# Kernel optimization log

Measured on AMD Instinct MI355X. Metric: run time of the kernel, lower is better.

The kernel has to match this reference:

```python
import jax, jax.numpy as jnp
import numpy as np

B = 5                      # dat_sz hardcoded in module; kernel shapes force batch == 5
X_DIM = 4096
H_DIM = 4096
T_DIM = 4096
D_DIM = X_DIM // T_DIM     # = 1 (required so z_dim == t_dim broadcasts in reparameterize_nm)
L_DIM = D_DIM * (D_DIM + 1) // 2
Z_DIM = T_DIM * L_DIM      # = 4096


def _linear_params(key, din, dout):
    kw, kb = jax.random.split(key)
    W = jax.random.normal(kw, (din, dout), dtype=jnp.float32) / np.float32(np.sqrt(din))
    b = jax.random.normal(kb, (dout,), dtype=jnp.float32) * np.float32(0.01)
    return W, b


def setup_inputs() -> dict:
    key = jax.random.key(0)
    ks = jax.random.split(key, 20)
    inp = {}
    inp["x"] = jax.random.normal(ks[0], (B, X_DIM), dtype=jnp.float32)
    inp["eps_xi"] = jax.random.normal(ks[1], (B, T_DIM), dtype=jnp.float32)
    inp["eps_f"] = jax.random.normal(ks[2], (B, D_DIM), dtype=jnp.float32)
    inp["eps_z"] = jax.random.normal(ks[3], (B, Z_DIM), dtype=jnp.float32)
    inp["W1"], inp["b1"] = _linear_params(ks[4], X_DIM, H_DIM)
    inp["W11"], inp["b11"] = _linear_params(ks[5], H_DIM, T_DIM)
    inp["W12"], inp["b12"] = _linear_params(ks[6], H_DIM, T_DIM)
    inp["W2"], inp["b2"] = _linear_params(ks[7], D_DIM, H_DIM)
    inp["W21"], inp["b21"] = _linear_params(ks[8], H_DIM, Z_DIM)
    inp["W22"], inp["b22"] = _linear_params(ks[9], H_DIM, T_DIM)
    inp["W23"], inp["b23"] = _linear_params(ks[10], X_DIM + Z_DIM, H_DIM)
    inp["W24"], inp["b24"] = _linear_params(ks[11], H_DIM, T_DIM + D_DIM)
    inp["W25"], inp["b25"] = _linear_params(ks[12], H_DIM, T_DIM + D_DIM)
    inp["W3"], inp["b3"] = _linear_params(ks[13], Z_DIM, H_DIM)
    inp["W31"], inp["b31"] = _linear_params(ks[14], H_DIM, X_DIM)
    inp["W32"], inp["b32"] = _linear_params(ks[15], H_DIM, X_DIM)
    inp["s"] = jax.random.normal(ks[16], (B, T_DIM), dtype=jnp.float32)
    inp["t"] = jax.random.normal(ks[17], (B, D_DIM), dtype=jnp.float32)
    inp["sigma"] = jnp.asarray(0.01, dtype=jnp.float32)
    inp["w"] = jnp.ones((T_DIM,), dtype=jnp.float32) / np.float32(T_DIM)
    inp["dist"] = 1  # unused by forward (matches torch signature)
    return inp


def _ard_kernel(a, b, sigma, w):
    # K[i,j] = sigma^2 * exp(-0.5 * sum_d w_d (a_i,d - b_j,d)^2)
    # Vectorized replacement of the original O(B^2) Python double loop.
    d2 = (a[:, None, :] - b[None, :, :]) ** 2            # [B, B, T]
    return (sigma ** 2) * jnp.exp(-0.5 * jnp.einsum('ijt,t->ij', d2, w))


def reference(x, eps_xi, eps_f, eps_z,
              W1, b1, W11, b11, W12, b12,
              W2, b2, W21, b21, W22, b22,
              W23, b23, W24, b24, W25, b25,
              W3, b3, W31, b31, W32, b32,
              s, t, sigma, w, dist):
    relu = jax.nn.relu
    # encode_1
    h1 = relu(x @ W1 + b1)
    qxi_mean = h1 @ W11 + b11
    log_qxi_cov = h1 @ W12 + b12
    # reparameterize_nm
    xi = jnp.exp(0.5 * log_qxi_cov) * eps_xi + qxi_mean
    # reparameterize_gp (training branch)
    K_ss = _ard_kernel(s, s, sigma, w)                    # [5,5]
    K_xs = _ard_kernel(xi, s, sigma, w)                   # [5,5]
    kk_inv = K_xs @ jnp.linalg.inv(K_ss)                  # [5,5]
    qf_mean = kk_inv @ t                                  # [5,D]
    cov = _ard_kernel(xi, xi, sigma, w) - kk_inv @ _ard_kernel(s, xi, sigma, w)
    qf_cov = jnp.diag(cov)                                # [5]
    f = jnp.sqrt(qf_cov)[:, None] * eps_f + qf_mean       # [5,D]
    # encode_2
    h2 = relu(f @ W2 + b2)
    z_mean = h2 @ W21 + b21                               # [5,Z]
    z_cov = h2 @ W22 + b22                                # [5,T] (== Z since d_dim=1)
    z = jnp.exp(0.5 * z_cov) * eps_z + z_mean
    # encode_3
    h23 = relu(jnp.concatenate([x, z], axis=1) @ W23 + b23)
    r_mean = h23 @ W24 + b24                              # [5,T+D]
    r_cov = h23 @ W25 + b25
    # decode
    h3 = relu(z @ W3 + b3)
    x_mean = h3 @ W31 + b31
    x_cov = h3 @ W32 + b32
    # losses
    qf_cov2 = jnp.broadcast_to(qf_cov[:, None], (B, D_DIM))
    q_mean = jnp.concatenate([qxi_mean, qf_mean], axis=1)
    q_cov = jnp.concatenate([log_qxi_cov, jnp.log(qf_cov2)], axis=1)
    kld1 = 0.5 * jnp.sum(-z_cov - 1.0 + jnp.exp(z_cov) + z_mean ** 2) / B
    kld2 = 0.5 * jnp.sum(r_cov - q_cov - 1.0
                         + jnp.exp(q_cov - r_cov)
                         + (q_mean - r_mean) ** 2 * jnp.exp(-r_cov)) / B
    kld_loss = kld1 + kld2
    log_pi = jnp.log(jnp.asarray(np.pi, dtype=jnp.float32))
    nll_loss = 0.5 * jnp.sum(log_pi + x_cov + jnp.exp(-x_cov) * (x - x_mean) ** 2) / B
    return (kld_loss, nll_loss, z_mean, z_cov, x_mean, x_cov)
```

## Files before the change

### kernel.cpp

```cpp
#include <hip/hip_runtime.h>
#include <math.h>

#define B5 5
#define DX 4096
#define DT 4096
#define DR 4097

enum {
  WS_SUMS  = 0,
  WS_CNT_XI  = 3,
  WS_CNT_FIN = 4,
  WS_CNT_ARD = 5,
  WS_ZERO_END = 8,
  WS_ACT1  = 16,
  WS_ACT23 = WS_ACT1  + 20480,
  WS_ACT3  = WS_ACT23 + 20480,
  WS_QXI_F = WS_ACT3  + 20480,
  WS_LQC_F = WS_QXI_F + 20480,
  WS_XIV   = WS_LQC_F + 20480,
  WS_Z     = WS_XIV   + 20480,
  WS_KSS   = WS_Z     + 20480,
  WS_KXS   = WS_KSS + 32,
  WS_F     = WS_KXS + 32,
  WS_QFM   = WS_F   + 8,
  WS_QFC   = WS_QFM + 8,
  WS_PART  = 143472,
  WS_P_H1  = WS_PART,
  WS_P_QXI = WS_P_H1  + 1310720,
  WS_P_LQC = WS_P_QXI + 1310720,
  WS_P_ZM  = WS_P_LQC + 1310720,
  WS_P_ZC  = WS_P_ZM  + 1310720,
  WS_P_H23 = WS_P_ZC  + 1310720,
  WS_P_H3  = WS_P_H23 + 2621440,
  WS_P_RM  = WS_P_H3  + 1310720,
  WS_P_RC  = WS_P_RM  + 1311040,
  WS_P_XM  = WS_P_RC  + 1311040,
  WS_P_XC  = WS_P_XM  + 1310720,
  WS_END   = WS_P_XC  + 1310720
};

#define GCOLS 256
#define GK    64
#define WROWS 16

__device__ inline float wave_sum(float v) {
  #pragma unroll
  for (int o = 32; o > 0; o >>= 1) v += __shfl_down(v, o, 64);
  return v;
}

template<int PROLOG, int DUAL, int ALIGNED>
__device__ __forceinline__ void gemm5_body(
    float* sx, float* red, int bx, int by,
    const float* __restrict__ p0, const float* __restrict__ p1,
    const float* __restrict__ p2,
    const float* __restrict__ Wa, const float* __restrict__ Wb,
    float* __restrict__ Pa,       float* __restrict__ Pb,
    int din, int dout)
{
  const int tid  = threadIdx.x;
  const int lane = tid & 63;
  const int wv   = tid >> 6;
  const long i0  = (long)by * GK;
  const long r0  = i0 + (long)wv * WROWS;

  float* sw = sx + wv * 80;
  for (int t = lane; t < B5 * WROWS; t += 64) {
    int b  = t >> 4;
    int il = t & 15;
    int i  = (int)(r0 + il);
    float v;
    if (PROLOG == 0)      v = p0[(long)b * din + i];
    else if (PROLOG == 2) v = fmaxf(p0[b] * p1[i] + p2[i], 0.f);
    else                  v = (i < DX) ? p0[(long)b * DX + i] : p1[(long)b * DT + (i - DX)];
    sw[t] = v;
  }

  const long o0 = (long)bx * GCOLS + lane * 4;
  const bool c0 = (o0 < dout), c1 = (o0 + 1 < dout), c2 = (o0 + 2 < dout), c3 = (o0 + 3 < dout);

  float accA[B5][4] = {};
  float accB[B5][4] = {};
  const float* wa = Wa + r0 * dout + o0;
  const float* wb = DUAL ? (Wb + r0 * dout + o0) : nullptr;

  #pragma unroll 8
  for (int il = 0; il < WROWS; ++il) {
    float4 A, Bv;
    if (ALIGNED) {
      A = *(const float4*)wa;
      if (DUAL) Bv = *(const float4*)wb;
    } else {
      A.x = c0 ? wa[0] : 0.f; A.y = c1 ? wa[1] : 0.f;
      A.z = c2 ? wa[2] : 0.f; A.w = c3 ? wa[3] : 0.f;
      if (DUAL) {
        Bv.x = c0 ? wb[0] : 0.f; Bv.y = c1 ? wb[1] : 0.f;
        Bv.z = c2 ? wb[2] : 0.f; Bv.w = c3 ? wb[3] : 0.f;
      }
    }
    #pragma unroll
    for (int b = 0; b < B5; ++b) {
      float xv = sw[b * WROWS + il];
      accA[b][0] += xv * A.x;  accA[b][1] += xv * A.y;
      accA[b][2] += xv * A.z;  accA[b][3] += xv * A.w;
      if (DUAL) {
        accB[b][0] += xv * Bv.x; accB[b][1] += xv * Bv.y;
        accB[b][2] += xv * Bv.z; accB[b][3] += xv * Bv.w;
      }
    }
    wa += dout; if (DUAL) wb += dout;
  }

  const int NJ = DUAL ? 40 : 20;
  if (wv > 0) {
    float* rr = red + (long)(wv - 1) * NJ * 64 + lane;
    #pragma unroll
    for (int b = 0; b < B5; ++b)
      #pragma unroll
      for (int j = 0; j < 4; ++j) {
        rr[(b*4+j)*64] = accA[b][j];
        if (DUAL) rr[(20+b*4+j)*64] = accB[b][j];
      }
  }
  __syncthreads();
  if (wv == 0) {
    #pragma unroll
    for (int w2 = 0; w2 < 3; ++w2) {
      const float* rr = red + (long)w2 * NJ * 64 + lane;
      #pragma unroll
      for (int b = 0; b < B5; ++b)
        #pragma unroll
        for (int j = 0; j < 4; ++j) {
          accA[b][j] += rr[(b*4+j)*64];
          if (DUAL) accB[b][j] += rr[(20+b*4+j)*64];
        }
    }
    if (c0) {
      #pragma unroll
      for (int b = 0; b < B5; ++b) {
        float* pa = Pa + ((long)by * B5 + b) * dout + o0;
        if (ALIGNED) *(float4*)pa = make_float4(accA[b][0], accA[b][1], accA[b][2], accA[b][3]);
        else { pa[0] = accA[b][0]; if (c1) pa[1] = accA[b][1];
               if (c2) pa[2] = accA[b][2]; if (c3) pa[3] = accA[b][3]; }
        if (DUAL) {
          float* pb = Pb + ((long)by * B5 + b) * dout + o0;
          if (ALIGNED) *(float4*)pb = make_float4(accB[b][0], accB[b][1], accB[b][2], accB[b][3]);
          else { pb[0] = accB[b][0]; if (c1) pb[1] = accB[b][1];
                 if (c2) pb[2] = accB[b][2]; if (c3) pb[3] = accB[b][3]; }
        }
      }
    }
  }
}

template<int PROLOG, int DUAL, int ALIGNED>
__global__ __launch_bounds__(256) void gemm5(
    const float* __restrict__ p0, const float* __restrict__ p1,
    const float* __restrict__ p2,
    const float* __restrict__ Wa, const float* __restrict__ Wb,
    float* __restrict__ Pa,       float* __restrict__ Pb,
    int din, int dout)
{
  __shared__ float sx[4 * 80];
  __shared__ float red[3 * 40 * 64];
  gemm5_body<PROLOG, DUAL, ALIGNED>(sx, red, blockIdx.x, blockIdx.y,
      p0, p1, p2, Wa, Wb, Pa, Pb, din, dout);
}

__global__ __launch_bounds__(256) void gemm5_G46(
    const float* __restrict__ x,   const float* __restrict__ z,
    const float* __restrict__ W23, float* __restrict__ P23,
    const float* __restrict__ W3,  float* __restrict__ P3)
{
  __shared__ float sx[4 * 80];
  __shared__ float red[3 * 40 * 64];
  int id = blockIdx.x;
  if (id < 2048) {
    gemm5_body<3, 0, 1>(sx, red, id & 15, id >> 4, x, z, nullptr,
                        W23, nullptr, P23, nullptr, 8192, 4096);
  } else {
    id -= 2048;
    gemm5_body<0, 0, 1>(sx, red, id & 15, id >> 4, z, nullptr, nullptr,
                        W3, nullptr, P3, nullptr, 4096, 4096);
  }
}

__global__ __launch_bounds__(256) void gemm5_G57(
    const float* __restrict__ act23,
    const float* __restrict__ W24, const float* __restrict__ W25,
    float* __restrict__ PRM,       float* __restrict__ PRC,
    const float* __restrict__ act3,
    const float* __restrict__ W31, const float* __restrict__ W32,
    float* __restrict__ PXM,       float* __restrict__ PXC)
{
  __shared__ float sx[4 * 80];
  __shared__ float red[3 * 40 * 64];
  int id = blockIdx.x;
  if (id < 1088) {
    gemm5_body<0, 1, 0>(sx, red, id % 17, id / 17, act23, nullptr, nullptr,
                        W24, W25, PRM, PRC, 4096, 4097);
  } else {
    id -= 1088;
    gemm5_body<0, 1, 1>(sx, red, id & 15, id >> 4, act3, nullptr, nullptr,
                        W31, W32, PXM, PXC, 4096, 4096);
  }
}

__global__ __launch_bounds__(256) void k_act1(
    const float* __restrict__ P, const float* __restrict__ bias, float* __restrict__ act,
    float* __restrict__ ctrl)
{
  if (blockIdx.x == 0 && threadIdx.x < WS_ZERO_END) ctrl[threadIdx.x] = 0.f;
  int idx = blockIdx.x * 256 + threadIdx.x;
  int b = idx >> 12, col = idx & (DT - 1);
  const float* pp = P + (long)b * DT + col;
  float s = 0.f;
  #pragma unroll 8
  for (int ks = 0; ks < 64; ++ks) s += pp[(long)ks * (B5 * DT)];
  act[idx] = fmaxf(s + bias[col], 0.f);
}

__global__ __launch_bounds__(256) void k_act23(
    const float* __restrict__ P23, const float* __restrict__ b23, float* __restrict__ act23,
    const float* __restrict__ P3,  const float* __restrict__ b3,  float* __restrict__ act3)
{
  int idx = blockIdx.x * 256 + threadIdx.x;
  if (idx < B5 * DT) {
    int b = idx >> 12, col = idx & (DT - 1);
    const float* pp = P23 + (long)b * DT + col;
    float s = 0.f;
    #pragma unroll 8
    for (int ks = 0; ks < 128; ++ks) s += pp[(long)ks * (B5 * DT)];
    act23[idx] = fmaxf(s + b23[col], 0.f);
  } else {
    int j = idx - B5 * DT;
    int b = j >> 12, col = j & (DT - 1);
    const float* pp = P3 + (long)b * DT + col;
    float s = 0.f;
    #pragma unroll 8
    for (int ks = 0; ks < 64; ++ks) s += pp[(long)ks * (B5 * DT)];
    act3[j] = fmaxf(s + b3[col], 0.f);
  }
}

__global__ __launch_bounds__(256) void k_xiard(
    const float* __restrict__ Pq, const float* __restrict__ Pl,
    const float* __restrict__ b11, const float* __restrict__ b12,
    const float* __restrict__ eps_xi,
    const float* __restrict__ s,   const float* __restrict__ w,
    const float* __restrict__ sigma,
    const float* __restrict__ t_in, const float* __restrict__ eps_f,
    float* __restrict__ qf, float* __restrict__ lf, float* __restrict__ xiv,
    float* __restrict__ Kss, float* __restrict__ Kxs,
    int* __restrict__ cnt_xi, int* __restrict__ cnt_ard,
    float* __restrict__ fv, float* __restrict__ qfm, float* __restrict__ qfc)
{
  if (blockIdx.x < 80) {
    int idx = blockIdx.x * 256 + threadIdx.x;
    int b = idx >> 12, col = idx & (DT - 1);
    const float* pq = Pq + (long)b * DT + col;
    const float* pl = Pl + (long)b * DT + col;
    float sq = 0.f, sl = 0.f;
    #pragma unroll 8
    for (int ks = 0; ks < 64; ++ks) { sq += pq[(long)ks * (B5 * DT)]; sl += pl[(long)ks * (B5 * DT)]; }
    float qm = sq + b11[col];
    float lq = sl + b12[col];
    qf[idx] = qm; lf[idx] = lq;
    xiv[idx] = expf(0.5f * lq) * eps_xi[idx] + qm;
    __threadfence();
    __syncthreads();
    if (threadIdx.x == 0) atomicAdd(cnt_xi, 1);
    return;
  }

  const int bid = blockIdx.x - 80;
  const bool xs = (bid >= 25);
  int q = xs ? bid - 25 : bid;
  const int i = q / 5, j = q % 5;

  if (xs) {
    if (threadIdx.x == 0) { while (atomicAdd(cnt_xi, 0) < 80) {} }
    __syncthreads();
    __threadfence();
  }
  const float* aa = xs ? (xiv + (long)i * DT) : (s + (long)i * DT);
  const float* bb = s + (long)j * DT;

  float sum = 0.f;
  for (int t = threadIdx.x; t < DT; t += 256) {
    float d = aa[t] - bb[t];
    sum += w[t] * d * d;
  }
  sum = wave_sum(sum);
  __shared__ float red[4];
  int lane = threadIdx.x & 63, wv = threadIdx.x >> 6;
  if (lane == 0) red[wv] = sum;
  __syncthreads();

  if (threadIdx.x == 0) {
    float tot = red[0] + red[1] + red[2] + red[3];
    float sg = sigma[0];
    float K = sg * sg * expf(-0.5f * tot);
    (xs ? Kxs : Kss)[i * 5 + j] = K;
    __threadfence();
    int old = atomicAdd(cnt_ard, 1);
    if (old == 49) {
      __threadfence();
      double M[5][5], Inv[5][5];
      for (int a = 0; a < 5; ++a)
        for (int b = 0; b < 5; ++b) { M[a][b] = Kss[a * 5 + b]; Inv[a][b] = (a == b) ? 1.0 : 0.0; }
      for (int c = 0; c < 5; ++c) {
        int p = c; double best = fabs(M[c][c]);
        for (int r = c + 1; r < 5; ++r) if (fabs(M[r][c]) > best) { best = fabs(M[r][c]); p = r; }
        if (p != c)
          for (int k = 0; k < 5; ++k) {
            double tm = M[c][k]; M[c][k] = M[p][k]; M[p][k] = tm;
            tm = Inv[c][k]; Inv[c][k] = Inv[p][k]; Inv[p][k] = tm;
          }
        double piv = 1.0 / M[c][c];
        for (int k = 0; k < 5; ++k) { M[c][k] *= piv; Inv[c][k] *= piv; }
        for (int r = 0; r < 5; ++r) if (r != c) {
          double m = M[r][c];
          for (int k = 0; k < 5; ++k) { M[r][k] -= m * M[c][k]; Inv[r][k] -= m * Inv[c][k]; }
        }
      }
      double kk[5][5];
      for (int a = 0; a < 5; ++a)
        for (int b = 0; b < 5; ++b) {
          double acc = 0.0;
          for (int k = 0; k < 5; ++k) acc += (double)Kxs[a * 5 + k] * Inv[k][b];
          kk[a][b] = acc;
        }
      double sg2 = (double)sg * (double)sg;
      for (int a = 0; a < 5; ++a) {
        double qm = 0.0, qc = sg2;
        for (int b = 0; b < 5; ++b) { qm += kk[a][b] * (double)t_in[b]; qc -= kk[a][b] * (double)Kxs[a * 5 + b]; }
        if (qc < 1e-12) qc = 1e-12;
        qfm[a] = (float)qm;
        qfc[a] = (float)qc;
        fv[a]  = sqrtf((float)qc) * eps_f[a] + (float)qm;
      }
    }
  }
}

__global__ __launch_bounds__(256) void k_z(
    const float* __restrict__ Pm, const float* __restrict__ Pc,
    const float* __restrict__ b21, const float* __restrict__ b22,
    const float* __restrict__ eps_z,
    float* __restrict__ out_zm, float* __restrict__ out_zc,
    float* __restrict__ zv, float* __restrict__ kld1sum)
{
  int idx = blockIdx.x * 256 + threadIdx.x;
  float term = 0.f;
  if (idx < B5 * DT) {
    int b = idx >> 12, col = idx & (DT - 1);
    const float* pm = Pm + (long)b * DT + col;
    const float* pc = Pc + (long)b * DT + col;
    float sm = 0.f, sc = 0.f;
    #pragma unroll 8
    for (int ks = 0; ks < 64; ++ks) { sm += pm[(long)ks * (B5 * DT)]; sc += pc[(long)ks * (B5 * DT)]; }
    float zm = sm + b21[col];
    float zc = sc + b22[col];
    out_zm[idx] = zm; out_zc[idx] = zc;
    zv[idx] = expf(0.5f * zc) * eps_z[idx] + zm;
    term = -zc - 1.f + expf(zc) + zm * zm;
  }
  term = wave_sum(term);
  if ((threadIdx.x & 63) == 0) atomicAdd(kld1sum, term);
}

__global__ __launch_bounds__(256) void k_fin(
    const float* __restrict__ Prm, const float* __restrict__ Prc,
    const float* __restrict__ b24, const float* __restrict__ b25,
    const float* __restrict__ qxi, const float* __restrict__ lqc,
    const float* __restrict__ qfm, const float* __restrict__ qfc,
    const float* __restrict__ Pxm, const float* __restrict__ Pxc,
    const float* __restrict__ b31, const float* __restrict__ b32,
    const float* __restrict__ x,
    float* __restrict__ out_xm, float* __restrict__ out_xc,
    float* __restrict__ sums, int* __restrict__ cnt, float* __restrict__ out01)
{
  const int gtid = blockIdx.x * 256 + threadIdx.x;
  float t2 = 0.f, t3 = 0.f;
  if (gtid < B5 * DR) {
    int b = gtid / DR, col = gtid % DR;
    const float* pm = Prm + (long)b * DR + col;
    const float* pc = Prc + (long)b * DR + col;
    float sm = 0.f, sc = 0.f;
    #pragma unroll 8
    for (int ks = 0; ks < 64; ++ks) { sm += pm[(long)ks * (B5 * DR)]; sc += pc[(long)ks * (B5 * DR)]; }
    float rm = sm + b24[col];
    float rc = sc + b25[col];
    float qm, qc;
    if (col < DT) { qm = qxi[(long)b * DT + col]; qc = lqc[(long)b * DT + col]; }
    else          { qm = qfm[b]; qc = logf(qfc[b]); }
    float d = qm - rm;
    t2 = rc - qc - 1.f + expf(qc - rc) + d * d * expf(-rc);
  } else {
    int idx = gtid - B5 * DR;
    if (idx < B5 * DX) {
      int b = idx >> 12, col = idx & (DX - 1);
      const float* pm = Pxm + (long)b * DX + col;
      const float* pc = Pxc + (long)b * DX + col;
      float sm = 0.f, sc = 0.f;
      #pragma unroll 8
      for (int ks = 0; ks < 64; ++ks) { sm += pm[(long)ks * (B5 * DX)]; sc += pc[(long)ks * (B5 * DX)]; }
      float xm = sm + b31[col];
      float xc = sc + b32[col];
      out_xm[idx] = xm; out_xc[idx] = xc;
      float d = x[idx] - xm;
      t3 = 1.14472988584940017f + xc + expf(-xc) * d * d;
    }
  }
  t2 = wave_sum(t2);
  t3 = wave_sum(t3);
  if ((threadIdx.x & 63) == 0) {
    if (t2 != 0.f) atomicAdd(&sums[1], t2);
    if (t3 != 0.f) atomicAdd(&sums[2], t3);
  }
  __syncthreads();
  if (threadIdx.x == 0) {
    __threadfence();
    int old = atomicAdd(cnt, 1);
    if (old == (int)gridDim.x - 1) {
      __threadfence();
      out01[0] = 0.5f * (sums[0] + sums[1]) / (float)B5;
      out01[1] = 0.5f * sums[2] / (float)B5;
    }
  }
}

extern "C" void kernel_launch(void* const* d_in, const int* in_sizes, int n_in,
                              void* d_out, int out_size, void* d_ws, size_t ws_size,
                              hipStream_t stream)
{
  const float* x      = (const float*)d_in[0];
  const float* eps_xi = (const float*)d_in[1];
  const float* eps_f  = (const float*)d_in[2];
  const float* eps_z  = (const float*)d_in[3];
  const float* W1  = (const float*)d_in[4];  const float* b1  = (const float*)d_in[5];
  const float* W11 = (const float*)d_in[6];  const float* b11 = (const float*)d_in[7];
  const float* W12 = (const float*)d_in[8];  const float* b12 = (const float*)d_in[9];
  const float* W2  = (const float*)d_in[10]; const float* b2  = (const float*)d_in[11];
  const float* W21 = (const float*)d_in[12]; const float* b21 = (const float*)d_in[13];
  const float* W22 = (const float*)d_in[14]; const float* b22 = (const float*)d_in[15];
  const float* W23 = (const float*)d_in[16]; const float* b23 = (const float*)d_in[17];
  const float* W24 = (const float*)d_in[18]; const float* b24 = (const float*)d_in[19];
  const float* W25 = (const float*)d_in[20]; const float* b25 = (const float*)d_in[21];
  const float* W3  = (const float*)d_in[22]; const float* b3  = (const float*)d_in[23];
  const float* W31 = (const float*)d_in[24]; const float* b31 = (const float*)d_in[25];
  const float* W32 = (const float*)d_in[26]; const float* b32 = (const float*)d_in[27];
  const float* s     = (const float*)d_in[28];
  const float* t     = (const float*)d_in[29];
  const float* sigma = (const float*)d_in[30];
  const float* w     = (const float*)d_in[31];

  float* ws  = (float*)d_ws;
  float* out = (float*)d_out;

  dim3 blk(256);

  gemm5<0,0,1><<<dim3(16,64), blk, 0, stream>>>(
      x, nullptr, nullptr, W1, nullptr, ws + WS_P_H1, nullptr, 4096, 4096);
  k_act1<<<80, blk, 0, stream>>>(ws + WS_P_H1, b1, ws + WS_ACT1, ws);
  gemm5<0,1,1><<<dim3(16,64), blk, 0, stream>>>(
      ws + WS_ACT1, nullptr, nullptr, W11, W12, ws + WS_P_QXI, ws + WS_P_LQC, 4096, 4096);
  k_xiard<<<130, blk, 0, stream>>>(
      ws + WS_P_QXI, ws + WS_P_LQC, b11, b12, eps_xi,
      s, w, sigma, t, eps_f,
      ws + WS_QXI_F, ws + WS_LQC_F, ws + WS_XIV,
      ws + WS_KSS, ws + WS_KXS,
      (int*)(ws + WS_CNT_XI), (int*)(ws + WS_CNT_ARD),
      ws + WS_F, ws + WS_QFM, ws + WS_QFC);
  gemm5<2,1,1><<<dim3(16,64), blk, 0, stream>>>(
      ws + WS_F, W2, b2, W21, W22, ws + WS_P_ZM, ws + WS_P_ZC, 4096, 4096);
  k_z<<<80, blk, 0, stream>>>(
      ws + WS_P_ZM, ws + WS_P_ZC, b21, b22, eps_z,
      out + 2, out + 2 + 20480, ws + WS_Z, ws + WS_SUMS);
  gemm5_G46<<<3072, blk, 0, stream>>>(
      x, ws + WS_Z, W23, ws + WS_P_H23, W3, ws + WS_P_H3);
  k_act23<<<160, blk, 0, stream>>>(
      ws + WS_P_H23, b23, ws + WS_ACT23, ws + WS_P_H3, b3, ws + WS_ACT3);
  gemm5_G57<<<2112, blk, 0, stream>>>(
      ws + WS_ACT23, W24, W25, ws + WS_P_RM, ws + WS_P_RC,
      ws + WS_ACT3,  W31, W32, ws + WS_P_XM, ws + WS_P_XC);
  k_fin<<<161, blk, 0, stream>>>(
      ws + WS_P_RM, ws + WS_P_RC, b24, b25,
      ws + WS_QXI_F, ws + WS_LQC_F,
      ws + WS_QFM, ws + WS_QFC,
      ws + WS_P_XM, ws + WS_P_XC, b31, b32, x,
      out + 2 + 40960, out + 2 + 61440,
      ws + WS_SUMS, (int*)(ws + WS_CNT_FIN), out);
}
```

Before: 257.5 us.

## Retile GEMV kernels to 16-row K slices with wider column tiles

Restructures the skinny batch-5 GEMM kernels. Each block now covers 16 K rows and 512 output columns, with each of the four waves owning 128 columns via float2 loads, instead of splitting K across waves and reducing through shared memory. This removes the LDS cross-wave reduction and its sync, and doubles the grid size. The cost is four times as many split-K partial sums, so the workspace grows and the downstream reduce kernels must read 256 or 512 partials per output instead of 64, which adds substantial memory traffic.

```diff
diff --git a/kernel.cpp b/kernel.cpp
--- a/kernel.cpp
+++ b/kernel.cpp
@@ -26,22 +26,21 @@
   WS_QFC   = WS_QFM + 8,
   WS_PART  = 143472,
   WS_P_H1  = WS_PART,
-  WS_P_QXI = WS_P_H1  + 1310720,
-  WS_P_LQC = WS_P_QXI + 1310720,
-  WS_P_ZM  = WS_P_LQC + 1310720,
-  WS_P_ZC  = WS_P_ZM  + 1310720,
-  WS_P_H23 = WS_P_ZC  + 1310720,
-  WS_P_H3  = WS_P_H23 + 2621440,
-  WS_P_RM  = WS_P_H3  + 1310720,
-  WS_P_RC  = WS_P_RM  + 1311040,
-  WS_P_XM  = WS_P_RC  + 1311040,
-  WS_P_XC  = WS_P_XM  + 1310720,
-  WS_END   = WS_P_XC  + 1310720
+  WS_P_QXI = WS_P_H1  + 5242880,
+  WS_P_LQC = WS_P_QXI + 5242880,
+  WS_P_ZM  = WS_P_LQC + 5242880,
+  WS_P_ZC  = WS_P_ZM  + 5242880,
+  WS_P_H23 = WS_P_ZC  + 5242880,
+  WS_P_H3  = WS_P_H23 + 10485760,
+  WS_P_RM  = WS_P_H3  + 5242880,
+  WS_P_RC  = WS_P_RM  + 5244160,
+  WS_P_XM  = WS_P_RC  + 5244160,
+  WS_P_XC  = WS_P_XM  + 5242880,
+  WS_END   = WS_P_XC  + 5242880
 };
 
-#define GCOLS 256
-#define GK    64
-#define WROWS 16
+#define GCOLS 512
+#define GK    16
 
 __device__ inline float wave_sum(float v) {
   #pragma unroll
@@ -51,7 +50,7 @@
 
 template<int PROLOG, int DUAL, int ALIGNED>
 __device__ __forceinline__ void gemm5_body(
-    float* sx, float* red, int bx, int by,
+    float* sx, int bx, int by,
     const float* __restrict__ p0, const float* __restrict__ p1,
     const float* __restrict__ p2,
     const float* __restrict__ Wa, const float* __restrict__ Wb,
@@ -62,92 +61,56 @@
   const int lane = tid & 63;
   const int wv   = tid >> 6;
   const long i0  = (long)by * GK;
-  const long r0  = i0 + (long)wv * WROWS;
-
-  float* sw = sx + wv * 80;
-  for (int t = lane; t < B5 * WROWS; t += 64) {
-    int b  = t >> 4;
-    int il = t & 15;
-    int i  = (int)(r0 + il);
+
+  if (tid < B5 * GK) {
+    int b  = tid >> 4;
+    int il = tid & 15;
+    int i  = (int)i0 + il;
     float v;
     if (PROLOG == 0)      v = p0[(long)b * din + i];
     else if (PROLOG == 2) v = fmaxf(p0[b] * p1[i] + p2[i], 0.f);
     else                  v = (i < DX) ? p0[(long)b * DX + i] : p1[(long)b * DT + (i - DX)];
-    sw[t] = v;
-  }
-
-  const long o0 = (long)bx * GCOLS + lane * 4;
-  const bool c0 = (o0 < dout), c1 = (o0 + 1 < dout), c2 = (o0 + 2 < dout), c3 = (o0 + 3 < dout);
-
-  float accA[B5][4] = {};
-  float accB[B5][4] = {};
-  const float* wa = Wa + r0 * dout + o0;
-  const float* wb = DUAL ? (Wb + r0 * dout + o0) : nullptr;
+    sx[b * GK + il] = v;
+  }
+  __syncthreads();
+
+  const long o0 = (long)bx * GCOLS + wv * 128 + lane * 2;
+  const bool c0 = (o0 < dout), c1 = (o0 + 1 < dout);
+
+  float accA[B5][2] = {};
+  float accB[B5][2] = {};
+  const float* wa = Wa + i0 * dout + o0;
+  const float* wb = DUAL ? (Wb + i0 * dout + o0) : nullptr;
 
   #pragma unroll 8
-  for (int il = 0; il < WROWS; ++il) {
-    float4 A, Bv;
+  for (int il = 0; il < GK; ++il) {
+    float w0a, w1a, w0b = 0.f, w1b = 0.f;
     if (ALIGNED) {
-      A = *(const float4*)wa;
-      if (DUAL) Bv = *(const float4*)wb;
+      float2 ta = *(const float2*)wa; w0a = ta.x; w1a = ta.y;
+      if (DUAL) { float2 tb = *(const float2*)wb; w0b = tb.x; w1b = tb.y; }
     } else {
-      A.x = c0 ? wa[0] : 0.f; A.y = c1 ? wa[1] : 0.f;
-      A.z = c2 ? wa[2] : 0.f; A.w = c3 ? wa[3] : 0.f;
-      if (DUAL) {
-        Bv.x = c0 ? wb[0] : 0.f; Bv.y = c1 ? wb[1] : 0.f;
-        Bv.z = c2 ? wb[2] : 0.f; Bv.w = c3 ? wb[3] : 0.f;
-      }
+      w0a = c0 ? wa[0] : 0.f; w1a = c1 ? wa[1] : 0.f;
+      if (DUAL) { w0b = c0 ? wb[0] : 0.f; w1b = c1 ? wb[1] : 0.f; }
     }
     #pragma unroll
     for (int b = 0; b < B5; ++b) {
-      float xv = sw[b * WROWS + il];
-      accA[b][0] += xv * A.x;  accA[b][1] += xv * A.y;
-      accA[b][2] += xv * A.z;  accA[b][3] += xv * A.w;
+      float xv = sx[b * GK + il];
+      accA[b][0] += xv * w0a; accA[b][1] += xv * w1a;
+      if (DUAL) { accB[b][0] += xv * w0b; accB[b][1] += xv * w1b; }
+    }
+    wa += dout; if (DUAL) wb += dout;
+  }
+
+  if (c0) {
+    #pragma unroll
+    for (int b = 0; b < B5; ++b) {
+      float* pa = Pa + ((long)by * B5 + b) * dout + o0;
+      if (ALIGNED) *(float2*)pa = make_float2(accA[b][0], accA[b][1]);
+      else { pa[0] = accA[b][0]; if (c1) pa[1] = accA[b][1]; }
       if (DUAL) {
-        accB[b][0] += xv * Bv.x; accB[b][1] += xv * Bv.y;
-        accB[b][2] += xv * Bv.z; accB[b][3] += xv * Bv.w;
-      }
-    }
-    wa += dout; if (DUAL) wb += dout;
-  }
-
-  const int NJ = DUAL ? 40 : 20;
-  if (wv > 0) {
-    float* rr = red + (long)(wv - 1) * NJ * 64 + lane;
-    #pragma unroll
-    for (int b = 0; b < B5; ++b)
-      #pragma unroll
-      for (int j = 0; j < 4; ++j) {
-        rr[(b*4+j)*64] = accA[b][j];
-        if (DUAL) rr[(20+b*4+j)*64] = accB[b][j];
-      }
-  }
-  __syncthreads();
-  if (wv == 0) {
-    #pragma unroll
-    for (int w2 = 0; w2 < 3; ++w2) {
-      const float* rr = red + (long)w2 * NJ * 64 + lane;
-      #pragma unroll
-      for (int b = 0; b < B5; ++b)
-        #pragma unroll
-        for (int j = 0; j < 4; ++j) {
-          accA[b][j] += rr[(b*4+j)*64];
-          if (DUAL) accB[b][j] += rr[(20+b*4+j)*64];
-        }
-    }
-    if (c0) {
-      #pragma unroll
-      for (int b = 0; b < B5; ++b) {
-        float* pa = Pa + ((long)by * B5 + b) * dout + o0;
-        if (ALIGNED) *(float4*)pa = make_float4(accA[b][0], accA[b][1], accA[b][2], accA[b][3]);
-        else { pa[0] = accA[b][0]; if (c1) pa[1] = accA[b][1];
-               if (c2) pa[2] = accA[b][2]; if (c3) pa[3] = accA[b][3]; }
-        if (DUAL) {
-          float* pb = Pb + ((long)by * B5 + b) * dout + o0;
-          if (ALIGNED) *(float4*)pb = make_float4(accB[b][0], accB[b][1], accB[b][2], accB[b][3]);
-          else { pb[0] = accB[b][0]; if (c1) pb[1] = accB[b][1];
-                 if (c2) pb[2] = accB[b][2]; if (c3) pb[3] = accB[b][3]; }
-        }
+        float* pb = Pb + ((long)by * B5 + b) * dout + o0;
+        if (ALIGNED) *(float2*)pb = make_float2(accB[b][0], accB[b][1]);
+        else { pb[0] = accB[b][0]; if (c1) pb[1] = accB[b][1]; }
       }
     }
   }
@@ -161,9 +124,8 @@
     float* __restrict__ Pa,       float* __restrict__ Pb,
     int din, int dout)
 {
-  __shared__ float sx[4 * 80];
-  __shared__ float red[3 * 40 * 64];
-  gemm5_body<PROLOG, DUAL, ALIGNED>(sx, red, blockIdx.x, blockIdx.y,
+  __shared__ float sx[B5 * GK];
+  gemm5_body<PROLOG, DUAL, ALIGNED>(sx, blockIdx.x, blockIdx.y,
       p0, p1, p2, Wa, Wb, Pa, Pb, din, dout);
 }
 
@@ -172,15 +134,14 @@
     const float* __restrict__ W23, float* __restrict__ P23,
     const float* __restrict__ W3,  float* __restrict__ P3)
 {
-  __shared__ float sx[4 * 80];
-  __shared__ float red[3 * 40 * 64];
+  __shared__ float sx[B5 * GK];
   int id = blockIdx.x;
-  if (id < 2048) {
-    gemm5_body<3, 0, 1>(sx, red, id & 15, id >> 4, x, z, nullptr,
+  if (id < 4096) {
+    gemm5_body<3, 0, 1>(sx, id & 7, id >> 3, x, z, nullptr,
                         W23, nullptr, P23, nullptr, 8192, 4096);
   } else {
-    id -= 2048;
-    gemm5_body<0, 0, 1>(sx, red, id & 15, id >> 4, z, nullptr, nullptr,
+    id -= 4096;
+    gemm5_body<0, 0, 1>(sx, id & 7, id >> 3, z, nullptr, nullptr,
                         W3, nullptr, P3, nullptr, 4096, 4096);
   }
 }
@@ -193,15 +154,14 @@
     const float* __restrict__ W31, const float* __restrict__ W32,
     float* __restrict__ PXM,       float* __restrict__ PXC)
 {
-  __shared__ float sx[4 * 80];
-  __shared__ float red[3 * 40 * 64];
+  __shared__ float sx[B5 * GK];
   int id = blockIdx.x;
-  if (id < 1088) {
-    gemm5_body<0, 1, 0>(sx, red, id % 17, id / 17, act23, nullptr, nullptr,
+  if (id < 2304) {
+    gemm5_body<0, 1, 0>(sx, id % 9, id / 9, act23, nullptr, nullptr,
                         W24, W25, PRM, PRC, 4096, 4097);
   } else {
-    id -= 1088;
-    gemm5_body<0, 1, 1>(sx, red, id & 15, id >> 4, act3, nullptr, nullptr,
+    id -= 2304;
+    gemm5_body<0, 1, 1>(sx, id & 7, id >> 3, act3, nullptr, nullptr,
                         W31, W32, PXM, PXC, 4096, 4096);
   }
 }
@@ -216,7 +176,7 @@
   const float* pp = P + (long)b * DT + col;
   float s = 0.f;
   #pragma unroll 8
-  for (int ks = 0; ks < 64; ++ks) s += pp[(long)ks * (B5 * DT)];
+  for (int ks = 0; ks < 256; ++ks) s += pp[(long)ks * (B5 * DT)];
   act[idx] = fmaxf(s + bias[col], 0.f);
 }
 
@@ -230,7 +190,7 @@
     const float* pp = P23 + (long)b * DT + col;
     float s = 0.f;
     #pragma unroll 8
-    for (int ks = 0; ks < 128; ++ks) s += pp[(long)ks * (B5 * DT)];
+    for (int ks = 0; ks < 512; ++ks) s += pp[(long)ks * (B5 * DT)];
     act23[idx] = fmaxf(s + b23[col], 0.f);
   } else {
     int j = idx - B5 * DT;
@@ -238,7 +198,7 @@
     const float* pp = P3 + (long)b * DT + col;
     float s = 0.f;
     #pragma unroll 8
-    for (int ks = 0; ks < 64; ++ks) s += pp[(long)ks * (B5 * DT)];
+    for (int ks = 0; ks < 256; ++ks) s += pp[(long)ks * (B5 * DT)];
     act3[j] = fmaxf(s + b3[col], 0.f);
   }
 }
@@ -262,7 +222,7 @@
     const float* pl = Pl + (long)b * DT + col;
     float sq = 0.f, sl = 0.f;
     #pragma unroll 8
-    for (int ks = 0; ks < 64; ++ks) { sq += pq[(long)ks * (B5 * DT)]; sl += pl[(long)ks * (B5 * DT)]; }
+    for (int ks = 0; ks < 256; ++ks) { sq += pq[(long)ks * (B5 * DT)]; sl += pl[(long)ks * (B5 * DT)]; }
     float qm = sq + b11[col];
     float lq = sl + b12[col];
     qf[idx] = qm; lf[idx] = lq;
@@ -359,7 +319,7 @@
     const float* pc = Pc + (long)b * DT + col;
     float sm = 0.f, sc = 0.f;
     #pragma unroll 8
-    for (int ks = 0; ks < 64; ++ks) { sm += pm[(long)ks * (B5 * DT)]; sc += pc[(long)ks * (B5 * DT)]; }
+    for (int ks = 0; ks < 256; ++ks) { sm += pm[(long)ks * (B5 * DT)]; sc += pc[(long)ks * (B5 * DT)]; }
     float zm = sm + b21[col];
     float zc = sc + b22[col];
     out_zm[idx] = zm; out_zc[idx] = zc;
@@ -389,7 +349,7 @@
     const float* pc = Prc + (long)b * DR + col;
     float sm = 0.f, sc = 0.f;
     #pragma unroll 8
-    for (int ks = 0; ks < 64; ++ks) { sm += pm[(long)ks * (B5 * DR)]; sc += pc[(long)ks * (B5 * DR)]; }
+    for (int ks = 0; ks < 256; ++ks) { sm += pm[(long)ks * (B5 * DR)]; sc += pc[(long)ks * (B5 * DR)]; }
     float rm = sm + b24[col];
     float rc = sc + b25[col];
     float qm, qc;
@@ -405,7 +365,7 @@
       const float* pc = Pxc + (long)b * DX + col;
       float sm = 0.f, sc = 0.f;
       #pragma unroll 8
-      for (int ks = 0; ks < 64; ++ks) { sm += pm[(long)ks * (B5 * DX)]; sc += pc[(long)ks * (B5 * DX)]; }
+      for (int ks = 0; ks < 256; ++ks) { sm += pm[(long)ks * (B5 * DX)]; sc += pc[(long)ks * (B5 * DX)]; }
       float xm = sm + b31[col];
       float xc = sc + b32[col];
       out_xm[idx] = xm; out_xc[idx] = xc;
@@ -461,10 +421,10 @@
 
   dim3 blk(256);
 
-  gemm5<0,0,1><<<dim3(16,64), blk, 0, stream>>>(
+  gemm5<0,0,1><<<dim3(8,256), blk, 0, stream>>>(
       x, nullptr, nullptr, W1, nullptr, ws + WS_P_H1, nullptr, 4096, 4096);
   k_act1<<<80, blk, 0, stream>>>(ws + WS_P_H1, b1, ws + WS_ACT1, ws);
-  gemm5<0,1,1><<<dim3(16,64), blk, 0, stream>>>(
+  gemm5<0,1,1><<<dim3(8,256), blk, 0, stream>>>(
       ws + WS_ACT1, nullptr, nullptr, W11, W12, ws + WS_P_QXI, ws + WS_P_LQC, 4096, 4096);
   k_xiard<<<130, blk, 0, stream>>>(
       ws + WS_P_QXI, ws + WS_P_LQC, b11, b12, eps_xi,
@@ -473,16 +433,16 @@
       ws + WS_KSS, ws + WS_KXS,
       (int*)(ws + WS_CNT_XI), (int*)(ws + WS_CNT_ARD),
       ws + WS_F, ws + WS_QFM, ws + WS_QFC);
-  gemm5<2,1,1><<<dim3(16,64), blk, 0, stream>>>(
+  gemm5<2,1,1><<<dim3(8,256), blk, 0, stream>>>(
       ws + WS_F, W2, b2, W21, W22, ws + WS_P_ZM, ws + WS_P_ZC, 4096, 4096);
   k_z<<<80, blk, 0, stream>>>(
       ws + WS_P_ZM, ws + WS_P_ZC, b21, b22, eps_z,
       out + 2, out + 2 + 20480, ws + WS_Z, ws + WS_SUMS);
-  gemm5_G46<<<3072, blk, 0, stream>>>(
+  gemm5_G46<<<6144, blk, 0, stream>>>(
       x, ws + WS_Z, W23, ws + WS_P_H23, W3, ws + WS_P_H3);
   k_act23<<<160, blk, 0, stream>>>(
       ws + WS_P_H23, b23, ws + WS_ACT23, ws + WS_P_H3, b3, ws + WS_ACT3);
-  gemm5_G57<<<2112, blk, 0, stream>>>(
+  gemm5_G57<<<4352, blk, 0, stream>>>(
       ws + WS_ACT23, W24, W25, ws + WS_P_RM, ws + WS_P_RC,
       ws + WS_ACT3,  W31, W32, ws + WS_P_XM, ws + WS_P_XC);
   k_fin<<<161, blk, 0, stream>>>(
```

Result: slower. 388.7 us (+50.9%).
